# Kernel tuning notes

Hardware: AMD Instinct MI355X
Metric: run time of the kernel (lower is better)

The kernel has to match this reference:

```python
import jax, jax.numpy as jnp
import numpy as np

BETA = 0.25  # init kwarg; exercises the 0 <= beta < 1 loss branch


def setup_inputs() -> dict:
    key = jax.random.key(0)
    k1, k2 = jax.random.split(key)
    N, D, K = 65536, 64, 4096
    x = jax.random.normal(k1, (N, D), dtype=jnp.float32)
    # original: uniform(-1/K, 1/K) then mean-centered; exact init distribution
    codebook = jax.random.uniform(k2, (K, D), dtype=jnp.float32,
                                  minval=-1.0 / K, maxval=1.0 / K)
    codebook = codebook - codebook.mean(axis=0, keepdims=True)
    return {"x": x, "codebook": codebook}


def reference(x, codebook):
    # pairwise squared distances via sum-of-squares + matmul: [N, K]
    dist = (jnp.sum(x * x, axis=1, keepdims=True)
            + jnp.sum(codebook * codebook, axis=1)
            - 2.0 * jnp.matmul(x, codebook.T))
    encoding_inds = jnp.argmin(dist, axis=1)            # [N]
    # gather codebook rows (equivalent to one-hot @ codebook, no one-hot materialized)
    quantized = jnp.take(codebook, encoding_inds, axis=0)  # [N, D]
    # straight-through estimator
    x_quantized = x + jax.lax.stop_gradient(quantized - x)
    mse = lambda a, b: jnp.mean((a - b) ** 2)
    loss = (BETA * mse(x, jax.lax.stop_gradient(quantized))
            + mse(quantized, jax.lax.stop_gradient(x)))
    return x_quantized, encoding_inds[:, None], loss
```

## Files before the change

### kernel.cpp

```cpp
#include <hip/hip_runtime.h>


#define D  64
#define NT 256

typedef unsigned short u16;
typedef short bf16x8 __attribute__((ext_vector_type(8)));
typedef float f32x4  __attribute__((ext_vector_type(4)));

#define VMWAIT_(n) asm volatile("s_waitcnt vmcnt(" #n ")" ::: "memory")
#define VMWAIT(n) VMWAIT_(n)

__device__ __forceinline__ u16 f32_to_bf16_raw(float f) {
    union { float f; unsigned u; } v; v.f = f;
    unsigned u = v.u;
    u += 0x7FFFu + ((u >> 16) & 1u);
    return (u16)(u >> 16);
}
__device__ __forceinline__ float bf16_raw_to_f32(u16 h) {
    union { unsigned u; float f; } v; v.u = ((unsigned)h) << 16;
    return v.f;
}
__device__ __forceinline__ f32x4 mfma16(bf16x8 a, bf16x8 b, f32x4 c) {
    return __builtin_amdgcn_mfma_f32_16x16x32_bf16(a, b, c, 0, 0, 0);
}

__device__ __forceinline__ float np_pairwise_sumsq_64(const float* p) {
    float r[8];
    #pragma unroll
    for (int j = 0; j < 8; ++j) r[j] = __fmul_rn(p[j], p[j]);
    #pragma unroll
    for (int i = 8; i < 64; i += 8) {
        #pragma unroll
        for (int j = 0; j < 8; ++j)
            r[j] = __fadd_rn(r[j], __fmul_rn(p[i + j], p[i + j]));
    }
    float t0 = __fadd_rn(r[0], r[1]);
    float t1 = __fadd_rn(r[2], r[3]);
    float t2 = __fadd_rn(r[4], r[5]);
    float t3 = __fadd_rn(r[6], r[7]);
    return __fadd_rn(__fadd_rn(t0, t1), __fadd_rn(t2, t3));
}

__global__ __launch_bounds__(256) void prep_kernel(const float* __restrict__ x,
                                                   const float* __restrict__ cb,
                                                   float* __restrict__ sx,
                                                   float* __restrict__ sc,
                                                   bf16x8* __restrict__ cbf,
                                                   int* __restrict__ amb_cnt) {
    int b = blockIdx.x;
    if (b == 0 && threadIdx.x == 0) *amb_cnt = 0;
    if (b < 272) {
        const float* a = (b < 256) ? x : cb;
        float* o = (b < 256) ? sx : sc;
        int r0 = (b < 256) ? b * 256 : (b - 256) * 256;
        int r = r0 + threadIdx.x;
        float buf[64];
        const float4* p = (const float4*)(a + (size_t)r * D);
        #pragma unroll
        for (int i = 0; i < 16; ++i) {
            float4 v = p[i];
            buf[4*i] = v.x; buf[4*i+1] = v.y; buf[4*i+2] = v.z; buf[4*i+3] = v.w;
        }
        o[r] = np_pairwise_sumsq_64(buf);
    } else {
        int t = b - 272;
        int tid = threadIdx.x;
        int lane = tid & 63;
        int ks = (tid >> 6) & 1;
        int hl = tid >> 7;
        int code = t * 16 + (lane & 15);
        int g = lane >> 4;
        bf16x8 v;
        #pragma unroll
        for (int j = 0; j < 8; ++j) {
            int d = ks * 32 + g * 4 + (j & 3) + 16 * (j >> 2);
            float val = cb[(size_t)code * D + d];
            u16 h = f32_to_bf16_raw(val);
            if (hl) {
                float resid = val - bf16_raw_to_f32(h);
                h = f32_to_bf16_raw(resid);
            }
            v[j] = (short)h;
        }
        cbf[((size_t)t * 4 + hl * 2 + ks) * 64 + lane] = v;
    }
}

#define MARG_A 1.6e-5f
#define MARG_B 6.5e-7f

#define STAGE(T, BUF) do {                                                    \
    const char* _src = (const char*)cbf + (size_t)(T) * 4096 + lane * 16;     \
    char* _dst = ringbase + (BUF) * 4096 + lane * 16;                         \
    __builtin_amdgcn_global_load_lds((const __attribute__((address_space(1))) unsigned int*)(_src),        (__attribute__((address_space(3))) unsigned int*)(_dst),        16, 0, 0); \
    __builtin_amdgcn_global_load_lds((const __attribute__((address_space(1))) unsigned int*)(_src + 1024), (__attribute__((address_space(3))) unsigned int*)(_dst + 1024), 16, 0, 0); \
    __builtin_amdgcn_global_load_lds((const __attribute__((address_space(1))) unsigned int*)(_src + 2048), (__attribute__((address_space(3))) unsigned int*)(_dst + 2048), 16, 0, 0); \
    __builtin_amdgcn_global_load_lds((const __attribute__((address_space(1))) unsigned int*)(_src + 3072), (__attribute__((address_space(3))) unsigned int*)(_dst + 3072), 16, 0, 0); \
} while (0)

#define DSREAD(T, BUF, SCK) do {                                              \
    const bf16x8* _bfr = (const bf16x8*)(ringbase + (BUF) * 4096);            \
    Fb0h = _bfr[lane]; Fb1h = _bfr[64 + lane];                                \
    Fb0l = _bfr[128 + lane]; Fb1l = _bfr[192 + lane];                         \
    SCK = scl[(T) * 16 + r];                                                  \
} while (0)

#define MFMAC(P) do {                                                         \
    _Pragma("unroll")                                                         \
    for (int s = 0; s < 4; ++s) {                                             \
        f32x4 _a = {0.f, 0.f, 0.f, 0.f};                                      \
        _a = mfma16(Ah0[s], Fb0h, _a);                                        \
        _a = mfma16(Ah1[s], Fb1h, _a);                                        \
        _a = mfma16(Ah0[s], Fb0l, _a);                                        \
        _a = mfma16(Ah1[s], Fb1l, _a);                                        \
        _a = mfma16(Al0[s], Fb0h, _a);                                        \
        _a = mfma16(Al1[s], Fb1h, _a);                                        \
        P[s] = _a;                                                            \
    }                                                                         \
} while (0)

#define VALUU(P, SCK, T) do {                                                 \
    int _kc = (T) * 16 + r;                                                   \
    _Pragma("unroll")                                                         \
    for (int s = 0; s < 4; ++s) {                                             \
        _Pragma("unroll")                                                     \
        for (int q = 0; q < 4; ++q) {                                         \
            int u = s * 4 + q;                                                \
            float sv = __fmaf_rn(-2.0f, P[s][q], SCK);                        \
            float m1o = m1[u];                                                \
            m2[u] = __builtin_amdgcn_fmed3f(sv, m1o, m2[u]);                  \
            i1[u] = (sv < m1o) ? _kc : i1[u];                                 \
            m1[u] = fminf(m1o, sv);                                           \
        }                                                                     \
    }                                                                         \
} while (0)

#define ITX(I, Pv, Sv, Pm, Sm, BR, BS) do {                                   \
    VMWAIT(4);                                                                \
    DSREAD(t0 + (I) + 1, BR, Sm);                                             \
    STAGE(t0 + (I) + 3, BS);                                                  \
    VALUU(Pv, Sv, t0 + (I));                                                  \
    MFMAC(Pm);                                                                \
} while (0)

__global__ __launch_bounds__(256) void phase1_kernel(
    const float* __restrict__ x, const float* __restrict__ sx,
    const float* __restrict__ sc, const bf16x8* __restrict__ cbf,
    int* __restrict__ idxbuf, int* __restrict__ amb_cnt, int* __restrict__ amb_rows)
{
    __shared__ __align__(16) char ring[4][3][4096];
    __shared__ float scl[4096];
    __shared__ float lm1[128][2], lm2[128][2];
    __shared__ int   li1[128][2];

    const int tid  = threadIdx.x;
    const int w    = tid >> 6;
    const int lane = tid & 63;
    const int r = lane & 15, g = lane >> 4;
    const int half = w & 1;
    const int rowg = w >> 1;
    const int wbase = blockIdx.x * 128 + rowg * 64;

    for (int j = tid; j < 1024; j += 256)
        *(float4*)&scl[j * 4] = *(const float4*)&sc[j * 4];
    __syncthreads();

    bf16x8 Ah0[4], Ah1[4], Al0[4], Al1[4];
    #pragma unroll
    for (int s = 0; s < 4; ++s) {
        const float* xr = x + (size_t)(wbase + s * 16 + r) * D;
        float e0[8], e1[8];
        float4 f0 = *(const float4*)(xr + g * 4);
        float4 f1 = *(const float4*)(xr + 16 + g * 4);
        float4 f2 = *(const float4*)(xr + 32 + g * 4);
        float4 f3 = *(const float4*)(xr + 48 + g * 4);
        e0[0]=f0.x;e0[1]=f0.y;e0[2]=f0.z;e0[3]=f0.w; e0[4]=f1.x;e0[5]=f1.y;e0[6]=f1.z;e0[7]=f1.w;
        e1[0]=f2.x;e1[1]=f2.y;e1[2]=f2.z;e1[3]=f2.w; e1[4]=f3.x;e1[5]=f3.y;e1[6]=f3.z;e1[7]=f3.w;
        #pragma unroll
        for (int j = 0; j < 8; ++j) {
            u16 h0 = f32_to_bf16_raw(e0[j]);
            Ah0[s][j] = (short)h0;
            Al0[s][j] = (short)f32_to_bf16_raw(e0[j] - bf16_raw_to_f32(h0));
            u16 h1 = f32_to_bf16_raw(e1[j]);
            Ah1[s][j] = (short)h1;
            Al1[s][j] = (short)f32_to_bf16_raw(e1[j] - bf16_raw_to_f32(h1));
        }
    }

    float m1[16], m2[16];
    int   i1[16];
    #pragma unroll
    for (int u = 0; u < 16; ++u) { m1[u] = 3.4e38f; m2[u] = 3.4e38f; i1[u] = 0; }

    const int t0 = half * 128;
    char* ringbase = &ring[w][0][0];

    bf16x8 Fb0h, Fb1h, Fb0l, Fb1l;
    f32x4  PA[4], PB[4];
    float  sA, sB;

    VMWAIT(0);
    STAGE(t0 + 0, 0); STAGE(t0 + 1, 1); STAGE(t0 + 2, 2);
    VMWAIT(8);
    DSREAD(t0 + 0, 0, sA);
    MFMAC(PA);

    #pragma unroll 1
    for (int i = 0; i < 120; i += 6) {
        ITX(i + 0, PA, sA, PB, sB, 1, 0);
        ITX(i + 1, PB, sB, PA, sA, 2, 1);
        ITX(i + 2, PA, sA, PB, sB, 0, 2);
        ITX(i + 3, PB, sB, PA, sA, 1, 0);
        ITX(i + 4, PA, sA, PB, sB, 2, 1);
        ITX(i + 5, PB, sB, PA, sA, 0, 2);
    }
    ITX(120, PA, sA, PB, sB, 1, 0);
    ITX(121, PB, sB, PA, sA, 2, 1);
    ITX(122, PA, sA, PB, sB, 0, 2);
    ITX(123, PB, sB, PA, sA, 1, 0);
    ITX(124, PA, sA, PB, sB, 2, 1);
    VMWAIT(4); DSREAD(t0 + 126, 0, sA); VALUU(PB, sB, t0 + 125); MFMAC(PA);
    VMWAIT(0); DSREAD(t0 + 127, 1, sB); VALUU(PA, sA, t0 + 126); MFMAC(PB);
    VALUU(PB, sB, t0 + 127);

    #pragma unroll
    for (int u = 0; u < 16; ++u) {
        #pragma unroll
        for (int mm = 1; mm < 16; mm <<= 1) {
            float om1 = __shfl_xor(m1[u], mm, 64);
            float om2 = __shfl_xor(m2[u], mm, 64);
            int   oi1 = __shfl_xor(i1[u], mm, 64);
            float nm2 = fminf(fmaxf(m1[u], om1), fminf(m2[u], om2));
            i1[u] = (om1 < m1[u]) ? oi1 : i1[u];
            m1[u] = fminf(m1[u], om1);
            m2[u] = nm2;
        }
    }
    if (r == 0) {
        #pragma unroll
        for (int u = 0; u < 16; ++u) {
            int rowin = rowg * 64 + (u >> 2) * 16 + g * 4 + (u & 3);
            lm1[rowin][half] = m1[u];
            lm2[rowin][half] = m2[u];
            li1[rowin][half] = i1[u];
        }
    }
    __syncthreads();

    if (tid < 128) {
        float a1 = lm1[tid][0], b1 = lm1[tid][1];
        float a2 = lm2[tid][0], b2 = lm2[tid][1];
        int   ia = li1[tid][0], ib = li1[tid][1];
        float m1f = fminf(a1, b1);
        float m2f = fminf(fmaxf(a1, b1), fminf(a2, b2));
        int   i1f = (b1 < a1) ? ib : ia;
        int orow = blockIdx.x * 128 + tid;
        idxbuf[orow] = i1f;
        float marg = __fmaf_rn(sx[orow], MARG_B, MARG_A);
        if (m2f - m1f <= marg) {
            int slot = atomicAdd(amb_cnt, 1);
            amb_rows[slot] = orow;
        }
    }
}

__global__ __launch_bounds__(256) void exact_scan(
    const float* __restrict__ x, const float* __restrict__ cb,
    const float* __restrict__ sx, const float* __restrict__ sc,
    const int* __restrict__ amb_cnt, const int* __restrict__ amb_rows,
    int* __restrict__ idxbuf)
{
    __shared__ float csT[4][64][64];
    __shared__ float xsT[64][16];
    __shared__ float redv[16][64];
    __shared__ int   redi[16][64];
    __shared__ float sxl[16];
    __shared__ int   rowids[16];

    const int tid = threadIdx.x;
    const int cnt = *amb_cnt;
    const int tz = tid >> 6, ty = (tid >> 4) & 3, cx = tid & 15;

    for (int base = blockIdx.x * 16; base < cnt; base += gridDim.x * 16) {
        if (tid < 16) {
            int i = base + tid;
            int rr = (i < cnt) ? amb_rows[i] : amb_rows[base];
            rowids[tid] = rr;
            sxl[tid] = sx[rr];
        }
        __syncthreads();
        {
            int rr = rowids[tid >> 4];
            int dg = tid & 15;
            float4 v = *(const float4*)(x + (size_t)rr * D + dg * 4);
            xsT[dg*4+0][tid>>4] = v.x; xsT[dg*4+1][tid>>4] = v.y;
            xsT[dg*4+2][tid>>4] = v.z; xsT[dg*4+3][tid>>4] = v.w;
        }

        float bv[4]; int bi[4];
        #pragma unroll
        for (int i = 0; i < 4; ++i) { bv[i] = 3.4e38f; bi[i] = 0x7fffffff; }

        for (int st = 0; st < 16; ++st) {
            __syncthreads();
            {
                int code = st * 256 + tid;
                const float4* src = (const float4*)(cb + (size_t)code * D);
                #pragma unroll
                for (int dd = 0; dd < 16; ++dd) {
                    float4 v = src[dd];
                    csT[tid>>6][dd*4+0][tid&63] = v.x; csT[tid>>6][dd*4+1][tid&63] = v.y;
                    csT[tid>>6][dd*4+2][tid&63] = v.z; csT[tid>>6][dd*4+3][tid&63] = v.w;
                }
            }
            __syncthreads();

            float acc[4][4];
            #pragma unroll
            for (int i = 0; i < 4; ++i)
                #pragma unroll
                for (int j = 0; j < 4; ++j) acc[i][j] = 0.0f;

            #pragma unroll 4
            for (int d = 0; d < 64; ++d) {
                float4 xv = *(const float4*)&xsT[d][ty * 4];
                float4 cv = *(const float4*)&csT[tz][d][cx * 4];
                float xr[4] = {xv.x, xv.y, xv.z, xv.w};
                float cc[4] = {cv.x, cv.y, cv.z, cv.w};
                #pragma unroll
                for (int i = 0; i < 4; ++i)
                    #pragma unroll
                    for (int j = 0; j < 4; ++j)
                        acc[i][j] = __fmaf_rn(xr[i], cc[j], acc[i][j]);
            }
            #pragma unroll
            for (int j = 0; j < 4; ++j) {
                int k = st * 256 + tz * 64 + cx * 4 + j;
                float sck = sc[k];
                #pragma unroll
                for (int i = 0; i < 4; ++i) {
                    float tt = __fadd_rn(sxl[ty * 4 + i], sck);
                    float u  = __fmul_rn(2.0f, acc[i][j]);
                    float s  = __fsub_rn(tt, u);
                    if (s < bv[i] || (s == bv[i] && k < bi[i])) { bv[i] = s; bi[i] = k; }
                }
            }
        }

        #pragma unroll
        for (int i = 0; i < 4; ++i) { redv[ty*4+i][tz*16+cx] = bv[i]; redi[ty*4+i][tz*16+cx] = bi[i]; }
        __syncthreads();
        if (tid < 16) {
            float bvv = redv[tid][0]; int bii = redi[tid][0];
            #pragma unroll 8
            for (int i = 1; i < 64; ++i) {
                float v = redv[tid][i]; int k = redi[tid][i];
                if (v < bvv || (v == bvv && k < bii)) { bvv = v; bii = k; }
            }
            idxbuf[rowids[tid]] = bii;
        }
        __syncthreads();
    }
}

__global__ __launch_bounds__(256) void finalize_rows(
    const float* __restrict__ x, const float* __restrict__ cb,
    const int* __restrict__ idxbuf,
    float* __restrict__ out_q, float* __restrict__ out_i,
    double* __restrict__ partials, int N)
{
    __shared__ double wsum[4];
    int wid = threadIdx.x >> 6, lane = threadIdx.x & 63;
    int n = blockIdx.x * 4 + wid;

    int idx = idxbuf[n];
    float q  = cb[(size_t)idx * D + lane];
    float xv = x[(size_t)n * D + lane];
    out_q[(size_t)n * D + lane] = q;

    double diff = (double)xv - (double)q;
    double s = diff * diff;
    #pragma unroll
    for (int off = 32; off > 0; off >>= 1) s += __shfl_down(s, off, 64);
    if (lane == 0) { wsum[wid] = s; out_i[n] = (float)idx; }
    __syncthreads();
    if (threadIdx.x == 0) partials[blockIdx.x] = (wsum[0] + wsum[1]) + (wsum[2] + wsum[3]);
}

__global__ __launch_bounds__(256) void loss_kernel(const double* __restrict__ partials,
                                                   int nP, float* __restrict__ out_loss,
                                                   double invND)
{
    __shared__ double red[256];
    double s = 0.0;
    for (int i = threadIdx.x; i < nP; i += 256) s += partials[i];
    red[threadIdx.x] = s;
    __syncthreads();
    #pragma unroll
    for (int step = 128; step > 0; step >>= 1) {
        if ((int)threadIdx.x < step) red[threadIdx.x] += red[threadIdx.x + step];
        __syncthreads();
    }
    if (threadIdx.x == 0) {
        double m = red[0] * invND;
        out_loss[0] = (float)(0.25 * m + m);
    }
}

extern "C" void kernel_launch(void* const* d_in, const int* in_sizes, int n_in,
                              void* d_out, int out_size, void* d_ws, size_t ws_size,
                              hipStream_t stream)
{
    const float* x  = (const float*)d_in[0];
    const float* cb = (const float*)d_in[1];
    const int N = in_sizes[0] / D;
    const int K = in_sizes[1] / D;

    float* out      = (float*)d_out;
    float* out_q    = out;
    float* out_i    = out + (size_t)N * D;
    float* out_loss = out_i + N;

    char* ws = (char*)d_ws;
    bf16x8* cbf      = (bf16x8*)ws;
    size_t off = (size_t)(K / 16) * 4 * 64 * sizeof(bf16x8);
    float*  sx       = (float*)(ws + off);  off += (size_t)N * 4;
    float*  sc       = (float*)(ws + off);  off += (size_t)K * 4;
    int*    idxbuf   = (int*)(ws + off);    off += (size_t)N * 4;
    int*    amb_rows = (int*)(ws + off);    off += (size_t)N * 4;
    double* partials = (double*)(ws + off); off += (size_t)(N / 4) * 8;
    int*    amb_cnt  = (int*)(ws + off);

    prep_kernel<<<272 + K / 16, 256, 0, stream>>>(x, cb, sx, sc, cbf, amb_cnt);
    phase1_kernel<<<N / 128, 256, 0, stream>>>(x, sx, sc, cbf, idxbuf, amb_cnt, amb_rows);
    exact_scan<<<1024, 256, 0, stream>>>(x, cb, sx, sc, amb_cnt, amb_rows, idxbuf);
    finalize_rows<<<N / 4, 256, 0, stream>>>(x, cb, idxbuf, out_q, out_i, partials, N);
    loss_kernel<<<1, 256, 0, stream>>>(partials, N / 4, out_loss,
                                       1.0 / ((double)N * (double)D));
}
```

Before: 248.5 us.

## Give each wave all codebook tiles over 32 rows instead of half-K split

```diff
diff --git a/kernel.cpp b/kernel.cpp
--- a/kernel.cpp
+++ b/kernel.cpp
@@ -108,7 +108,7 @@
 
 #define MFMAC(P) do {                                                         \
     _Pragma("unroll")                                                         \
-    for (int s = 0; s < 4; ++s) {                                             \
+    for (int s = 0; s < 2; ++s) {                                             \
         f32x4 _a = {0.f, 0.f, 0.f, 0.f};                                      \
         _a = mfma16(Ah0[s], Fb0h, _a);                                        \
         _a = mfma16(Ah1[s], Fb1h, _a);                                        \
@@ -123,7 +123,7 @@
 #define VALUU(P, SCK, T) do {                                                 \
     int _kc = (T) * 16 + r;                                                   \
     _Pragma("unroll")                                                         \
-    for (int s = 0; s < 4; ++s) {                                             \
+    for (int s = 0; s < 2; ++s) {                                             \
         _Pragma("unroll")                                                     \
         for (int q = 0; q < 4; ++q) {                                         \
             int u = s * 4 + q;                                                \
@@ -138,37 +138,33 @@
 
 #define ITX(I, Pv, Sv, Pm, Sm, BR, BS) do {                                   \
     VMWAIT(4);                                                                \
-    DSREAD(t0 + (I) + 1, BR, Sm);                                             \
-    STAGE(t0 + (I) + 3, BS);                                                  \
-    VALUU(Pv, Sv, t0 + (I));                                                  \
+    DSREAD((I) + 1, BR, Sm);                                                  \
+    STAGE((I) + 3, BS);                                                       \
+    VALUU(Pv, Sv, (I));                                                       \
     MFMAC(Pm);                                                                \
 } while (0)
 
-__global__ __launch_bounds__(256) void phase1_kernel(
+__global__ __launch_bounds__(256, 2) void phase1_kernel(
     const float* __restrict__ x, const float* __restrict__ sx,
     const float* __restrict__ sc, const bf16x8* __restrict__ cbf,
     int* __restrict__ idxbuf, int* __restrict__ amb_cnt, int* __restrict__ amb_rows)
 {
     __shared__ __align__(16) char ring[4][3][4096];
     __shared__ float scl[4096];
-    __shared__ float lm1[128][2], lm2[128][2];
-    __shared__ int   li1[128][2];
 
     const int tid  = threadIdx.x;
     const int w    = tid >> 6;
     const int lane = tid & 63;
     const int r = lane & 15, g = lane >> 4;
-    const int half = w & 1;
-    const int rowg = w >> 1;
-    const int wbase = blockIdx.x * 128 + rowg * 64;
+    const int wbase = blockIdx.x * 128 + w * 32;
 
     for (int j = tid; j < 1024; j += 256)
         *(float4*)&scl[j * 4] = *(const float4*)&sc[j * 4];
     __syncthreads();
 
-    bf16x8 Ah0[4], Ah1[4], Al0[4], Al1[4];
-    #pragma unroll
-    for (int s = 0; s < 4; ++s) {
+    bf16x8 Ah0[2], Ah1[2], Al0[2], Al1[2];
+    #pragma unroll
+    for (int s = 0; s < 2; ++s) {
         const float* xr = x + (size_t)(wbase + s * 16 + r) * D;
         float e0[8], e1[8];
         float4 f0 = *(const float4*)(xr + g * 4);
@@ -188,26 +184,25 @@
         }
     }
 
-    float m1[16], m2[16];
-    int   i1[16];
-    #pragma unroll
-    for (int u = 0; u < 16; ++u) { m1[u] = 3.4e38f; m2[u] = 3.4e38f; i1[u] = 0; }
-
-    const int t0 = half * 128;
+    float m1[8], m2[8];
+    int   i1[8];
+    #pragma unroll
+    for (int u = 0; u < 8; ++u) { m1[u] = 3.4e38f; m2[u] = 3.4e38f; i1[u] = 0; }
+
     char* ringbase = &ring[w][0][0];
 
     bf16x8 Fb0h, Fb1h, Fb0l, Fb1l;
-    f32x4  PA[4], PB[4];
+    f32x4  PA[2], PB[2];
     float  sA, sB;
 
     VMWAIT(0);
-    STAGE(t0 + 0, 0); STAGE(t0 + 1, 1); STAGE(t0 + 2, 2);
+    STAGE(0, 0); STAGE(1, 1); STAGE(2, 2);
     VMWAIT(8);
-    DSREAD(t0 + 0, 0, sA);
+    DSREAD(0, 0, sA);
     MFMAC(PA);
 
     #pragma unroll 1
-    for (int i = 0; i < 120; i += 6) {
+    for (int i = 0; i < 252; i += 6) {
         ITX(i + 0, PA, sA, PB, sB, 1, 0);
         ITX(i + 1, PB, sB, PA, sA, 2, 1);
         ITX(i + 2, PA, sA, PB, sB, 0, 2);
@@ -215,17 +210,13 @@
         ITX(i + 4, PA, sA, PB, sB, 2, 1);
         ITX(i + 5, PB, sB, PA, sA, 0, 2);
     }
-    ITX(120, PA, sA, PB, sB, 1, 0);
-    ITX(121, PB, sB, PA, sA, 2, 1);
-    ITX(122, PA, sA, PB, sB, 0, 2);
-    ITX(123, PB, sB, PA, sA, 1, 0);
-    ITX(124, PA, sA, PB, sB, 2, 1);
-    VMWAIT(4); DSREAD(t0 + 126, 0, sA); VALUU(PB, sB, t0 + 125); MFMAC(PA);
-    VMWAIT(0); DSREAD(t0 + 127, 1, sB); VALUU(PA, sA, t0 + 126); MFMAC(PB);
-    VALUU(PB, sB, t0 + 127);
-
-    #pragma unroll
-    for (int u = 0; u < 16; ++u) {
+    ITX(252, PA, sA, PB, sB, 1, 0);
+    VMWAIT(4); DSREAD(254, 2, sA); VALUU(PB, sB, 253); MFMAC(PA);
+    VMWAIT(0); DSREAD(255, 0, sB); VALUU(PA, sA, 254); MFMAC(PB);
+    VALUU(PB, sB, 255);
+
+    #pragma unroll
+    for (int u = 0; u < 8; ++u) {
         #pragma unroll
         for (int mm = 1; mm < 16; mm <<= 1) {
             float om1 = __shfl_xor(m1[u], mm, 64);
@@ -239,28 +230,14 @@
     }
     if (r == 0) {
         #pragma unroll
-        for (int u = 0; u < 16; ++u) {
-            int rowin = rowg * 64 + (u >> 2) * 16 + g * 4 + (u & 3);
-            lm1[rowin][half] = m1[u];
-            lm2[rowin][half] = m2[u];
-            li1[rowin][half] = i1[u];
-        }
-    }
-    __syncthreads();
-
-    if (tid < 128) {
-        float a1 = lm1[tid][0], b1 = lm1[tid][1];
-        float a2 = lm2[tid][0], b2 = lm2[tid][1];
-        int   ia = li1[tid][0], ib = li1[tid][1];
-        float m1f = fminf(a1, b1);
-        float m2f = fminf(fmaxf(a1, b1), fminf(a2, b2));
-        int   i1f = (b1 < a1) ? ib : ia;
-        int orow = blockIdx.x * 128 + tid;
-        idxbuf[orow] = i1f;
-        float marg = __fmaf_rn(sx[orow], MARG_B, MARG_A);
-        if (m2f - m1f <= marg) {
-            int slot = atomicAdd(amb_cnt, 1);
-            amb_rows[slot] = orow;
+        for (int u = 0; u < 8; ++u) {
+            int orow = wbase + (u >> 2) * 16 + g * 4 + (u & 3);
+            idxbuf[orow] = i1[u];
+            float marg = __fmaf_rn(sx[orow], MARG_B, MARG_A);
+            if (m2[u] - m1[u] <= marg) {
+                int slot = atomicAdd(amb_cnt, 1);
+                amb_rows[slot] = orow;
+            }
         }
     }
 }
```

Measured after the change: 288.7 us. 16.2% more time.

## Transpose MFMA operands so each lane reduces codebook entries per row

Applied to the files above, without the earlier changes.

```diff
diff --git a/kernel.cpp b/kernel.cpp
--- a/kernel.cpp
+++ b/kernel.cpp
@@ -99,52 +99,57 @@
     __builtin_amdgcn_global_load_lds((const __attribute__((address_space(1))) unsigned int*)(_src + 3072), (__attribute__((address_space(3))) unsigned int*)(_dst + 3072), 16, 0, 0); \
 } while (0)
 
-#define DSREAD(T, BUF, SCK) do {                                              \
+#define DSREAD(BUF) do {                                                      \
     const bf16x8* _bfr = (const bf16x8*)(ringbase + (BUF) * 4096);            \
     Fb0h = _bfr[lane]; Fb1h = _bfr[64 + lane];                                \
     Fb0l = _bfr[128 + lane]; Fb1l = _bfr[192 + lane];                         \
-    SCK = scl[(T) * 16 + r];                                                  \
 } while (0)
 
-#define MFMAC(P) do {                                                         \
+#define MFMAC() do {                                                          \
     _Pragma("unroll")                                                         \
     for (int s = 0; s < 4; ++s) {                                             \
         f32x4 _a = {0.f, 0.f, 0.f, 0.f};                                      \
-        _a = mfma16(Ah0[s], Fb0h, _a);                                        \
-        _a = mfma16(Ah1[s], Fb1h, _a);                                        \
-        _a = mfma16(Ah0[s], Fb0l, _a);                                        \
-        _a = mfma16(Ah1[s], Fb1l, _a);                                        \
-        _a = mfma16(Al0[s], Fb0h, _a);                                        \
-        _a = mfma16(Al1[s], Fb1h, _a);                                        \
+        _a = mfma16(Fb0h, Ah0[s], _a);                                        \
+        _a = mfma16(Fb1h, Ah1[s], _a);                                        \
+        _a = mfma16(Fb0l, Ah0[s], _a);                                        \
+        _a = mfma16(Fb1l, Ah1[s], _a);                                        \
+        _a = mfma16(Fb0h, Al0[s], _a);                                        \
+        _a = mfma16(Fb1h, Al1[s], _a);                                        \
         P[s] = _a;                                                            \
     }                                                                         \
 } while (0)
 
-#define VALUU(P, SCK, T) do {                                                 \
-    int _kc = (T) * 16 + r;                                                   \
+#define VALUU(T) do {                                                         \
+    f32x4 _sck = *(const f32x4*)&scl[(T) * 16 + g4];                          \
+    int _kb = (T) * 16 + g4;                                                  \
     _Pragma("unroll")                                                         \
     for (int s = 0; s < 4; ++s) {                                             \
-        _Pragma("unroll")                                                     \
-        for (int q = 0; q < 4; ++q) {                                         \
-            int u = s * 4 + q;                                                \
-            float sv = __fmaf_rn(-2.0f, P[s][q], SCK);                        \
-            float m1o = m1[u];                                                \
-            m2[u] = __builtin_amdgcn_fmed3f(sv, m1o, m2[u]);                  \
-            i1[u] = (sv < m1o) ? _kc : i1[u];                                 \
-            m1[u] = fminf(m1o, sv);                                           \
-        }                                                                     \
+        float _s0 = __fmaf_rn(-2.0f, P[s][0], _sck[0]);                       \
+        float _s1 = __fmaf_rn(-2.0f, P[s][1], _sck[1]);                       \
+        float _s2 = __fmaf_rn(-2.0f, P[s][2], _sck[2]);                       \
+        float _s3 = __fmaf_rn(-2.0f, P[s][3], _sck[3]);                       \
+        float _lo1 = fminf(_s0, _s1), _hi1 = fmaxf(_s0, _s1);                 \
+        float _lo2 = fminf(_s2, _s3), _hi2 = fmaxf(_s2, _s3);                 \
+        int _il1 = (_s1 < _s0) ? 1 : 0;                                       \
+        int _il2 = (_s3 < _s2) ? 3 : 2;                                       \
+        float _m1p = fminf(_lo1, _lo2);                                       \
+        int _ip = (_lo2 < _lo1) ? _il2 : _il1;                                \
+        float _m2p = fminf(fmaxf(_lo1, _lo2), fminf(_hi1, _hi2));             \
+        m2[s] = fminf(__builtin_amdgcn_fmed3f(_m1p, m1[s], m2[s]), _m2p);     \
+        i1[s] = (_m1p < m1[s]) ? (_kb + _ip) : i1[s];                         \
+        m1[s] = fminf(m1[s], _m1p);                                           \
     }                                                                         \
 } while (0)
 
-#define ITX(I, Pv, Sv, Pm, Sm, BR, BS) do {                                   \
-    VMWAIT(4);                                                                \
-    DSREAD(t0 + (I) + 1, BR, Sm);                                             \
+#define ITER(I, BS, BR) do {                                                  \
+    MFMAC();                                                                  \
     STAGE(t0 + (I) + 3, BS);                                                  \
-    VALUU(Pv, Sv, t0 + (I));                                                  \
-    MFMAC(Pm);                                                                \
+    VMWAIT(8);                                                                \
+    DSREAD(BR);                                                               \
+    VALUU(t0 + (I));                                                          \
 } while (0)
 
-__global__ __launch_bounds__(256) void phase1_kernel(
+__global__ __launch_bounds__(256, 2) void phase1_kernel(
     const float* __restrict__ x, const float* __restrict__ sx,
     const float* __restrict__ sc, const bf16x8* __restrict__ cbf,
     int* __restrict__ idxbuf, int* __restrict__ amb_cnt, int* __restrict__ amb_rows)
@@ -158,6 +163,7 @@
     const int w    = tid >> 6;
     const int lane = tid & 63;
     const int r = lane & 15, g = lane >> 4;
+    const int g4 = g * 4;
     const int half = w & 1;
     const int rowg = w >> 1;
     const int wbase = blockIdx.x * 128 + rowg * 64;
@@ -188,62 +194,54 @@
         }
     }
 
-    float m1[16], m2[16];
-    int   i1[16];
-    #pragma unroll
-    for (int u = 0; u < 16; ++u) { m1[u] = 3.4e38f; m2[u] = 3.4e38f; i1[u] = 0; }
+    float m1[4], m2[4];
+    int   i1[4];
+    #pragma unroll
+    for (int s = 0; s < 4; ++s) { m1[s] = 3.4e38f; m2[s] = 3.4e38f; i1[s] = 0; }
 
     const int t0 = half * 128;
     char* ringbase = &ring[w][0][0];
 
     bf16x8 Fb0h, Fb1h, Fb0l, Fb1l;
-    f32x4  PA[4], PB[4];
-    float  sA, sB;
+    f32x4  P[4];
 
     VMWAIT(0);
     STAGE(t0 + 0, 0); STAGE(t0 + 1, 1); STAGE(t0 + 2, 2);
     VMWAIT(8);
-    DSREAD(t0 + 0, 0, sA);
-    MFMAC(PA);
+    DSREAD(0);
 
     #pragma unroll 1
-    for (int i = 0; i < 120; i += 6) {
-        ITX(i + 0, PA, sA, PB, sB, 1, 0);
-        ITX(i + 1, PB, sB, PA, sA, 2, 1);
-        ITX(i + 2, PA, sA, PB, sB, 0, 2);
-        ITX(i + 3, PB, sB, PA, sA, 1, 0);
-        ITX(i + 4, PA, sA, PB, sB, 2, 1);
-        ITX(i + 5, PB, sB, PA, sA, 0, 2);
-    }
-    ITX(120, PA, sA, PB, sB, 1, 0);
-    ITX(121, PB, sB, PA, sA, 2, 1);
-    ITX(122, PA, sA, PB, sB, 0, 2);
-    ITX(123, PB, sB, PA, sA, 1, 0);
-    ITX(124, PA, sA, PB, sB, 2, 1);
-    VMWAIT(4); DSREAD(t0 + 126, 0, sA); VALUU(PB, sB, t0 + 125); MFMAC(PA);
-    VMWAIT(0); DSREAD(t0 + 127, 1, sB); VALUU(PA, sA, t0 + 126); MFMAC(PB);
-    VALUU(PB, sB, t0 + 127);
-
-    #pragma unroll
-    for (int u = 0; u < 16; ++u) {
-        #pragma unroll
-        for (int mm = 1; mm < 16; mm <<= 1) {
-            float om1 = __shfl_xor(m1[u], mm, 64);
-            float om2 = __shfl_xor(m2[u], mm, 64);
-            int   oi1 = __shfl_xor(i1[u], mm, 64);
-            float nm2 = fminf(fmaxf(m1[u], om1), fminf(m2[u], om2));
-            i1[u] = (om1 < m1[u]) ? oi1 : i1[u];
-            m1[u] = fminf(m1[u], om1);
-            m2[u] = nm2;
-        }
-    }
-    if (r == 0) {
-        #pragma unroll
-        for (int u = 0; u < 16; ++u) {
-            int rowin = rowg * 64 + (u >> 2) * 16 + g * 4 + (u & 3);
-            lm1[rowin][half] = m1[u];
-            lm2[rowin][half] = m2[u];
-            li1[rowin][half] = i1[u];
+    for (int i = 0; i < 123; i += 3) {
+        ITER(i + 0, 0, 1);
+        ITER(i + 1, 1, 2);
+        ITER(i + 2, 2, 0);
+    }
+    ITER(123, 0, 1);
+    ITER(124, 1, 2);
+    MFMAC(); VMWAIT(4); DSREAD(0); VALUU(t0 + 125);
+    MFMAC(); VMWAIT(0); DSREAD(1); VALUU(t0 + 126);
+    MFMAC(); VALUU(t0 + 127);
+
+    #pragma unroll
+    for (int s = 0; s < 4; ++s) {
+        #pragma unroll
+        for (int mm = 16; mm < 64; mm <<= 1) {
+            float om1 = __shfl_xor(m1[s], mm, 64);
+            float om2 = __shfl_xor(m2[s], mm, 64);
+            int   oi1 = __shfl_xor(i1[s], mm, 64);
+            float nm2 = fminf(fmaxf(m1[s], om1), fminf(m2[s], om2));
+            i1[s] = (om1 < m1[s]) ? oi1 : i1[s];
+            m1[s] = fminf(m1[s], om1);
+            m2[s] = nm2;
+        }
+    }
+    if (lane < 16) {
+        #pragma unroll
+        for (int s = 0; s < 4; ++s) {
+            int rowin = rowg * 64 + s * 16 + lane;
+            lm1[rowin][half] = m1[s];
+            lm2[rowin][half] = m2[s];
+            li1[rowin][half] = i1[s];
         }
     }
     __syncthreads();
```

New measurement: 243.6 us (median of 2 runs). 1.02x faster.
